# Kernel optimization log

Measured on AMD Instinct MI355X. Metric: run time of the kernel, lower is better.

Reference implementation:

```python
import jax, jax.numpy as jnp
import numpy as np

N_NODES = 4096
N_EDGES = 131072
C_IN = 256
C_OUT = 256
N_HEADS = 4
ALPHA = 0.2
NEG_FILL = -9e15


def setup_inputs() -> dict:
    key = jax.random.key(0)
    k_x, k_e, k_w, k_b, k_a = jax.random.split(key, 5)
    x = jax.random.normal(k_x, (N_NODES, C_IN), dtype=jnp.float32)
    edge_index = jax.random.randint(k_e, (2, N_EDGES), 0, N_NODES, dtype=jnp.int64)
    # nn.Linear(c_in, c_out): weight [c_out, c_in], bias [c_out]
    W = jax.random.normal(k_w, (C_OUT, C_IN), dtype=jnp.float32) * 0.05
    b = jax.random.normal(k_b, (C_OUT,), dtype=jnp.float32) * 0.05
    # attention vector a: [num_heads, 2 * c_out_per_head]
    a = jax.random.normal(k_a, (N_HEADS, 2 * (C_OUT // N_HEADS)), dtype=jnp.float32) * 0.05
    return {"x": x, "edge_index": edge_index, "W": W, "b": b, "a": a}


def reference(x, edge_index, W, b, a):
    N = x.shape[0]
    H = a.shape[0]
    C = W.shape[0] // H  # per-head feature dim

    # Linear projection then split heads: [N, H, C]
    feats = (x @ W.T + b).reshape(N, H, C)

    # Dense adjacency (faithful to the original index_select/scatter construction)
    adj = jnp.zeros((N, N), dtype=bool).at[edge_index[0], edge_index[1]].set(True)

    # attn_logits = leaky_relu(einsum('bhc,hc->bh', cat(f_i, f_j), a))
    # is separable: score(i,j,h) = leaky_relu(f_i . a[:, :C] + f_j . a[:, C:])
    s_src = jnp.einsum('nhc,hc->nh', feats, a[:, :C])  # [N, H]
    s_dst = jnp.einsum('nhc,hc->nh', feats, a[:, C:])  # [N, H]
    logits = jax.nn.leaky_relu(s_src[:, None, :] + s_dst[None, :, :], ALPHA)  # [N, N, H]

    masked = jnp.where(adj[..., None], logits, NEG_FILL)
    probs = jax.nn.softmax(masked, axis=1)  # softmax over source nodes j (dim=2 with batch)

    # Weighted aggregation: einsum('bijh,bjhc->bihc') then concat heads
    out = jnp.einsum('ijh,jhc->ihc', probs, feats).reshape(N, H * C)
    return out[None]  # [1, N, c_out] (batch_size = 1 in the original)
```

## Files before the change

kernel.cpp:

```cpp
#include <hip/hip_runtime.h>
#include <hip/hip_bf16.h>
#include <stdint.h>

#define N_NODES 4096
#define N_EDGES 131072
#define C_IN 256
#define C_OUT 256
#define N_HEADS 4
#define C_HEAD 64
#define MAX_DEG 128

typedef __attribute__((ext_vector_type(8))) short short8;
typedef __attribute__((ext_vector_type(4))) short short4v;
typedef __attribute__((ext_vector_type(4))) float floatx4;

union f32u { float f; uint32_t u; };
__device__ __forceinline__ float bf2f(short s) {
    f32u v; v.u = ((uint32_t)(uint16_t)s) << 16; return v.f;
}
__device__ __forceinline__ short f2bf(float f) {
    __hip_bfloat16 h = __float2bfloat16(f);
    return *reinterpret_cast<short*>(&h);
}

__global__ void scatter_edges(const int* __restrict__ ei,
                              unsigned short* __restrict__ nbr,
                              int* __restrict__ deg) {
    int e = blockIdx.x * blockDim.x + threadIdx.x;
    if (e >= N_EDGES) return;
    bool is64 = true;
    #pragma unroll
    for (int q = 1; q < 64; q += 2) is64 = is64 && (ei[q] == 0);
    int row, col;
    if (is64) {
        const long long* e64 = (const long long*)ei;
        row = (int)e64[e];
        col = (int)e64[N_EDGES + e];
    } else {
        row = ei[e];
        col = ei[N_EDGES + e];
    }
    int pos = atomicAdd(&deg[row], 1);
    if (pos < MAX_DEG) nbr[row * MAX_DEG + pos] = (unsigned short)col;
}

__global__ __launch_bounds__(256) void gemm_feats(
    const float* __restrict__ x, const float* __restrict__ W,
    const float* __restrict__ b, __hip_bfloat16* __restrict__ feats)
{
    int tid  = threadIdx.x;
    int lane = tid & 63;
    int wave = tid >> 6;
    int tile = blockIdx.x * 4 + wave;
    int row0 = (tile >> 4) * 16;
    int col0 = (tile & 15) * 16;
    int r    = lane & 15;
    int quad = lane >> 4;

    const floatx4* ax = (const floatx4*)(x + (size_t)(row0 + r) * C_IN);
    const floatx4* bw = (const floatx4*)(W + (size_t)(col0 + r) * C_IN);

    floatx4 acc = {0.f, 0.f, 0.f, 0.f};
    #pragma unroll
    for (int k8 = 0; k8 < 8; ++k8) {
        floatx4 a0 = ax[k8 * 8 + quad * 2], a1 = ax[k8 * 8 + quad * 2 + 1];
        floatx4 b0 = bw[k8 * 8 + quad * 2], b1 = bw[k8 * 8 + quad * 2 + 1];
        short8 av, bq;
        #pragma unroll
        for (int j = 0; j < 4; ++j) {
            av[j] = f2bf(a0[j]); av[4 + j] = f2bf(a1[j]);
            bq[j] = f2bf(b0[j]); bq[4 + j] = f2bf(b1[j]);
        }
        acc = __builtin_amdgcn_mfma_f32_16x16x32_bf16(av, bq, acc, 0, 0, 0);
    }

    int gn = col0 + r;
    float bias = b[gn];
    #pragma unroll
    for (int rr = 0; rr < 4; ++rr) {
        int gm = row0 + quad * 4 + rr;
        feats[(size_t)gm * C_OUT + gn] = __float2bfloat16(acc[rr] + bias);
    }
}

__global__ __launch_bounds__(64) void score_kernel(
    const __hip_bfloat16* __restrict__ feats, const float* __restrict__ a,
    float* __restrict__ s_src, float* __restrict__ s_dst)
{
    int gid = blockIdx.x * 64 + threadIdx.x;
    int n = gid >> 2, h = gid & 3;
    const short8*  f  = (const short8*)(feats + (size_t)n * C_OUT + h * C_HEAD);
    const floatx4* as = (const floatx4*)(a + h * 2 * C_HEAD);
    float ss = 0.f, sd = 0.f;
    #pragma unroll
    for (int v = 0; v < 8; ++v) {
        short8 fv = f[v];
        floatx4 s0 = as[v * 2],      s1 = as[v * 2 + 1];
        floatx4 d0 = as[16 + v * 2], d1 = as[16 + v * 2 + 1];
        #pragma unroll
        for (int j = 0; j < 4; ++j) {
            float x0 = bf2f(fv[j]);
            float x1 = bf2f(fv[4 + j]);
            ss += x0 * s0[j] + x1 * s1[j];
            sd += x0 * d0[j] + x1 * d1[j];
        }
    }
    s_src[gid] = ss;
    s_dst[gid] = sd;
}

__global__ __launch_bounds__(256) void aggregate(
    const unsigned short* __restrict__ nbr,
    const int* __restrict__ deg,
    const __hip_bfloat16* __restrict__ feats,
    const float* __restrict__ s_src,
    const float* __restrict__ s_dst,
    float* __restrict__ out)
{
    int i    = blockIdx.x;
    int t    = threadIdx.x;
    int wv   = t >> 6;
    int lane = t & 63;
    int h    = lane >> 4;

    __shared__ unsigned short lst[MAX_DEG];
    __shared__ unsigned char  ok[MAX_DEG];
    __shared__ float          wk[MAX_DEG][N_HEADS];
    __shared__ floatx4        red[4][64];

    int n = deg[i];
    n = (n < MAX_DEG) ? n : MAX_DEG;

    if (t < n) lst[t] = nbr[i * MAX_DEG + t];
    __syncthreads();
    if (t < n) {
        unsigned short v = lst[t];
        bool keep = true;
        for (int q = 0; q < t; ++q) keep = keep && (lst[q] != v);
        ok[t] = keep ? 1 : 0;
    }
    __syncthreads();
    for (int p = t; p < n * N_HEADS; p += 256) {
        int k = p >> 2, hh = p & 3;
        float l = s_src[i * N_HEADS + hh] + s_dst[(int)lst[k] * N_HEADS + hh];
        l = (l > 0.f) ? l : 0.2f * l;
        l = fminf(l, 60.f);
        wk[k][hh] = ok[k] ? __expf(l) : 0.f;
    }
    __syncthreads();

    floatx4 acc = {0.f, 0.f, 0.f, 0.f};
    if (n > 0) {
        for (int k = wv; k < n; k += 4) {
            float w = wk[k][h];
            short4v fv = *(const short4v*)(feats + (size_t)lst[k] * C_OUT + lane * 4);
            acc[0] += w * bf2f(fv[0]);
            acc[1] += w * bf2f(fv[1]);
            acc[2] += w * bf2f(fv[2]);
            acc[3] += w * bf2f(fv[3]);
        }
    } else {
        for (int j = wv; j < N_NODES; j += 4) {
            short4v fv = *(const short4v*)(feats + (size_t)j * C_OUT + lane * 4);
            acc[0] += bf2f(fv[0]);
            acc[1] += bf2f(fv[1]);
            acc[2] += bf2f(fv[2]);
            acc[3] += bf2f(fv[3]);
        }
    }
    red[wv][lane] = acc;
    __syncthreads();

    if (wv == 0) {
        floatx4 r0 = red[0][lane], r1 = red[1][lane], r2 = red[2][lane], r3 = red[3][lane];
        float denom;
        if (n > 0) {
            denom = 0.f;
            for (int k = 0; k < n; ++k) denom += wk[k][h];
            if (denom <= 0.f) denom = 1.f;
        } else {
            denom = (float)N_NODES;
        }
        float inv = 1.0f / denom;
        floatx4 o;
        o[0] = (r0[0] + r1[0] + r2[0] + r3[0]) * inv;
        o[1] = (r0[1] + r1[1] + r2[1] + r3[1]) * inv;
        o[2] = (r0[2] + r1[2] + r2[2] + r3[2]) * inv;
        o[3] = (r0[3] + r1[3] + r2[3] + r3[3]) * inv;
        *(floatx4*)(out + (size_t)i * C_OUT + lane * 4) = o;
    }
}

extern "C" void kernel_launch(void* const* d_in, const int* in_sizes, int n_in,
                              void* d_out, int out_size, void* d_ws, size_t ws_size,
                              hipStream_t stream) {
    const float* x  = (const float*)d_in[0];
    const int*   ei = (const int*)d_in[1];
    const float* W  = (const float*)d_in[2];
    const float* b  = (const float*)d_in[3];
    const float* a  = (const float*)d_in[4];
    float* out = (float*)d_out;

    uint8_t* ws = (uint8_t*)d_ws;
    __hip_bfloat16* feats = (__hip_bfloat16*)ws;
    unsigned short* nbr   = (unsigned short*)(ws + (2u << 20));
    int*            deg   = (int*)(ws + (3u << 20));
    float*          s_src = (float*)(ws + (3u << 20) + (16u << 10));
    float*          s_dst = (float*)(ws + (3u << 20) + (80u << 10));

    hipMemsetAsync(deg, 0, N_NODES * sizeof(int), stream);
    scatter_edges<<<N_EDGES / 256, 256, 0, stream>>>(ei, nbr, deg);
    gemm_feats<<<(N_NODES / 16) * (C_OUT / 16) / 4, 256, 0, stream>>>(x, W, b, feats);
    score_kernel<<<N_NODES * N_HEADS / 64, 64, 0, stream>>>(feats, a, s_src, s_dst);
    aggregate<<<N_NODES, 256, 0, stream>>>(nbr, deg, feats, s_src, s_dst, out);
}
```

Before: 111.2 us.

## Fuse GEMM with edge scatter and compute attention scores inside aggregation

Merges the edge-scatter and projection GEMM into one launch by splitting the block range between the two roles, with scatter blocks handling four edges per thread. The separate score kernel and its s_src/s_dst buffers are removed; the aggregate kernel now computes destination scores on the fly from the neighbour feature rows it already loads, using 16-lane shuffle reductions. The softmax denominator is accumulated per wave instead of in a serial loop over shared weights. This cuts two kernel launches and the shared-memory weight pass, at the cost of extra shuffles and dot products in the gather loop.

```diff
diff --git a/kernel.cpp b/kernel.cpp
--- a/kernel.cpp
+++ b/kernel.cpp
@@ -9,6 +9,8 @@
 #define N_HEADS 4
 #define C_HEAD 64
 #define MAX_DEG 128
+#define GEMM_BLOCKS 1024
+#define SCAT_BLOCKS 128
 
 typedef __attribute__((ext_vector_type(8))) short short8;
 typedef __attribute__((ext_vector_type(4))) short short4v;
@@ -23,98 +25,74 @@
     return *reinterpret_cast<short*>(&h);
 }
 
-__global__ void scatter_edges(const int* __restrict__ ei,
-                              unsigned short* __restrict__ nbr,
-                              int* __restrict__ deg) {
-    int e = blockIdx.x * blockDim.x + threadIdx.x;
-    if (e >= N_EDGES) return;
-    bool is64 = true;
-    #pragma unroll
-    for (int q = 1; q < 64; q += 2) is64 = is64 && (ei[q] == 0);
-    int row, col;
-    if (is64) {
-        const long long* e64 = (const long long*)ei;
-        row = (int)e64[e];
-        col = (int)e64[N_EDGES + e];
+__global__ __launch_bounds__(256) void k1_gemm_scatter(
+    const float* __restrict__ x, const float* __restrict__ W,
+    const float* __restrict__ b, const int* __restrict__ ei,
+    unsigned short* __restrict__ nbr, int* __restrict__ deg,
+    __hip_bfloat16* __restrict__ feats)
+{
+    int blk = blockIdx.x;
+    int tid = threadIdx.x;
+    if (blk < GEMM_BLOCKS) {
+        int lane = tid & 63;
+        int wave = tid >> 6;
+        int tile = blk * 4 + wave;
+        int row0 = (tile >> 4) * 16;
+        int col0 = (tile & 15) * 16;
+        int r    = lane & 15;
+        int quad = lane >> 4;
+
+        const floatx4* ax = (const floatx4*)(x + (size_t)(row0 + r) * C_IN);
+        const floatx4* bw = (const floatx4*)(W + (size_t)(col0 + r) * C_IN);
+
+        floatx4 acc = {0.f, 0.f, 0.f, 0.f};
+        #pragma unroll
+        for (int k8 = 0; k8 < 8; ++k8) {
+            floatx4 a0 = ax[k8 * 8 + quad * 2], a1 = ax[k8 * 8 + quad * 2 + 1];
+            floatx4 b0 = bw[k8 * 8 + quad * 2], b1 = bw[k8 * 8 + quad * 2 + 1];
+            short8 av, bq;
+            #pragma unroll
+            for (int j = 0; j < 4; ++j) {
+                av[j] = f2bf(a0[j]); av[4 + j] = f2bf(a1[j]);
+                bq[j] = f2bf(b0[j]); bq[4 + j] = f2bf(b1[j]);
+            }
+            acc = __builtin_amdgcn_mfma_f32_16x16x32_bf16(av, bq, acc, 0, 0, 0);
+        }
+        int gn = col0 + r;
+        float bias = b[gn];
+        #pragma unroll
+        for (int rr = 0; rr < 4; ++rr) {
+            int gm = row0 + quad * 4 + rr;
+            feats[(size_t)gm * C_OUT + gn] = __float2bfloat16(acc[rr] + bias);
+        }
     } else {
-        row = ei[e];
-        col = ei[N_EDGES + e];
-    }
-    int pos = atomicAdd(&deg[row], 1);
-    if (pos < MAX_DEG) nbr[row * MAX_DEG + pos] = (unsigned short)col;
-}
-
-__global__ __launch_bounds__(256) void gemm_feats(
-    const float* __restrict__ x, const float* __restrict__ W,
-    const float* __restrict__ b, __hip_bfloat16* __restrict__ feats)
-{
-    int tid  = threadIdx.x;
-    int lane = tid & 63;
-    int wave = tid >> 6;
-    int tile = blockIdx.x * 4 + wave;
-    int row0 = (tile >> 4) * 16;
-    int col0 = (tile & 15) * 16;
-    int r    = lane & 15;
-    int quad = lane >> 4;
-
-    const floatx4* ax = (const floatx4*)(x + (size_t)(row0 + r) * C_IN);
-    const floatx4* bw = (const floatx4*)(W + (size_t)(col0 + r) * C_IN);
-
-    floatx4 acc = {0.f, 0.f, 0.f, 0.f};
-    #pragma unroll
-    for (int k8 = 0; k8 < 8; ++k8) {
-        floatx4 a0 = ax[k8 * 8 + quad * 2], a1 = ax[k8 * 8 + quad * 2 + 1];
-        floatx4 b0 = bw[k8 * 8 + quad * 2], b1 = bw[k8 * 8 + quad * 2 + 1];
-        short8 av, bq;
-        #pragma unroll
-        for (int j = 0; j < 4; ++j) {
-            av[j] = f2bf(a0[j]); av[4 + j] = f2bf(a1[j]);
-            bq[j] = f2bf(b0[j]); bq[4 + j] = f2bf(b1[j]);
-        }
-        acc = __builtin_amdgcn_mfma_f32_16x16x32_bf16(av, bq, acc, 0, 0, 0);
-    }
-
-    int gn = col0 + r;
-    float bias = b[gn];
-    #pragma unroll
-    for (int rr = 0; rr < 4; ++rr) {
-        int gm = row0 + quad * 4 + rr;
-        feats[(size_t)gm * C_OUT + gn] = __float2bfloat16(acc[rr] + bias);
-    }
-}
-
-__global__ __launch_bounds__(64) void score_kernel(
-    const __hip_bfloat16* __restrict__ feats, const float* __restrict__ a,
-    float* __restrict__ s_src, float* __restrict__ s_dst)
-{
-    int gid = blockIdx.x * 64 + threadIdx.x;
-    int n = gid >> 2, h = gid & 3;
-    const short8*  f  = (const short8*)(feats + (size_t)n * C_OUT + h * C_HEAD);
-    const floatx4* as = (const floatx4*)(a + h * 2 * C_HEAD);
-    float ss = 0.f, sd = 0.f;
-    #pragma unroll
-    for (int v = 0; v < 8; ++v) {
-        short8 fv = f[v];
-        floatx4 s0 = as[v * 2],      s1 = as[v * 2 + 1];
-        floatx4 d0 = as[16 + v * 2], d1 = as[16 + v * 2 + 1];
-        #pragma unroll
-        for (int j = 0; j < 4; ++j) {
-            float x0 = bf2f(fv[j]);
-            float x1 = bf2f(fv[4 + j]);
-            ss += x0 * s0[j] + x1 * s1[j];
-            sd += x0 * d0[j] + x1 * d1[j];
-        }
-    }
-    s_src[gid] = ss;
-    s_dst[gid] = sd;
+        bool is64 = true;
+        #pragma unroll
+        for (int q = 1; q < 64; q += 2) is64 = is64 && (ei[q] == 0);
+        int base = (blk - GEMM_BLOCKS) * 256 + tid;
+        #pragma unroll
+        for (int qq = 0; qq < 4; ++qq) {
+            int e = base + qq * (SCAT_BLOCKS * 256);
+            int row, col;
+            if (is64) {
+                const long long* e64 = (const long long*)ei;
+                row = (int)e64[e];
+                col = (int)e64[N_EDGES + e];
+            } else {
+                row = ei[e];
+                col = ei[N_EDGES + e];
+            }
+            int pos = atomicAdd(&deg[row], 1);
+            if (pos < MAX_DEG) nbr[row * MAX_DEG + pos] = (unsigned short)col;
+        }
+    }
 }
 
 __global__ __launch_bounds__(256) void aggregate(
     const unsigned short* __restrict__ nbr,
     const int* __restrict__ deg,
     const __hip_bfloat16* __restrict__ feats,
-    const float* __restrict__ s_src,
-    const float* __restrict__ s_dst,
+    const float* __restrict__ a,
     float* __restrict__ out)
 {
     int i    = blockIdx.x;
@@ -122,11 +100,13 @@
     int wv   = t >> 6;
     int lane = t & 63;
     int h    = lane >> 4;
+    int li   = lane & 15;
 
     __shared__ unsigned short lst[MAX_DEG];
     __shared__ unsigned char  ok[MAX_DEG];
-    __shared__ float          wk[MAX_DEG][N_HEADS];
-    __shared__ floatx4        red[4][64];
+    __shared__ float          ssrc_sh[N_HEADS];
+    __shared__ floatx4        redv[4][64];
+    __shared__ float          redd[4][64];
 
     int n = deg[i];
     n = (n < MAX_DEG) ? n : MAX_DEG;
@@ -139,49 +119,59 @@
         for (int q = 0; q < t; ++q) keep = keep && (lst[q] != v);
         ok[t] = keep ? 1 : 0;
     }
+
+    floatx4 as4 = *(const floatx4*)(a + h * 2 * C_HEAD + 4 * li);
+    floatx4 ad4 = *(const floatx4*)(a + h * 2 * C_HEAD + C_HEAD + 4 * li);
+
+    if (wv == 0) {
+        short4v fi = *(const short4v*)(feats + (size_t)i * C_OUT + lane * 4);
+        float p = bf2f(fi[0]) * as4[0] + bf2f(fi[1]) * as4[1]
+                + bf2f(fi[2]) * as4[2] + bf2f(fi[3]) * as4[3];
+        p += __shfl_xor(p, 1, 16);
+        p += __shfl_xor(p, 2, 16);
+        p += __shfl_xor(p, 4, 16);
+        p += __shfl_xor(p, 8, 16);
+        if (li == 0) ssrc_sh[h] = p;
+    }
     __syncthreads();
-    for (int p = t; p < n * N_HEADS; p += 256) {
-        int k = p >> 2, hh = p & 3;
-        float l = s_src[i * N_HEADS + hh] + s_dst[(int)lst[k] * N_HEADS + hh];
-        l = (l > 0.f) ? l : 0.2f * l;
-        l = fminf(l, 60.f);
-        wk[k][hh] = ok[k] ? __expf(l) : 0.f;
-    }
-    __syncthreads();
-
+
+    float ssrc = ssrc_sh[h];
     floatx4 acc = {0.f, 0.f, 0.f, 0.f};
+    float   den = 0.f;
+
     if (n > 0) {
         for (int k = wv; k < n; k += 4) {
-            float w = wk[k][h];
-            short4v fv = *(const short4v*)(feats + (size_t)lst[k] * C_OUT + lane * 4);
-            acc[0] += w * bf2f(fv[0]);
-            acc[1] += w * bf2f(fv[1]);
-            acc[2] += w * bf2f(fv[2]);
-            acc[3] += w * bf2f(fv[3]);
+            int j = lst[k];
+            short4v fv = *(const short4v*)(feats + (size_t)j * C_OUT + lane * 4);
+            float f0 = bf2f(fv[0]), f1 = bf2f(fv[1]), f2 = bf2f(fv[2]), f3 = bf2f(fv[3]);
+            float p = f0 * ad4[0] + f1 * ad4[1] + f2 * ad4[2] + f3 * ad4[3];
+            p += __shfl_xor(p, 1, 16);
+            p += __shfl_xor(p, 2, 16);
+            p += __shfl_xor(p, 4, 16);
+            p += __shfl_xor(p, 8, 16);
+            float l = ssrc + p;
+            l = (l > 0.f) ? l : 0.2f * l;
+            float w = ok[k] ? __expf(fminf(l, 60.f)) : 0.f;
+            den += w;
+            acc[0] += w * f0; acc[1] += w * f1; acc[2] += w * f2; acc[3] += w * f3;
         }
     } else {
         for (int j = wv; j < N_NODES; j += 4) {
             short4v fv = *(const short4v*)(feats + (size_t)j * C_OUT + lane * 4);
-            acc[0] += bf2f(fv[0]);
-            acc[1] += bf2f(fv[1]);
-            acc[2] += bf2f(fv[2]);
-            acc[3] += bf2f(fv[3]);
-        }
-    }
-    red[wv][lane] = acc;
+            acc[0] += bf2f(fv[0]); acc[1] += bf2f(fv[1]);
+            acc[2] += bf2f(fv[2]); acc[3] += bf2f(fv[3]);
+            den += 1.0f;
+        }
+    }
+    redv[wv][lane] = acc;
+    redd[wv][lane] = den;
     __syncthreads();
 
     if (wv == 0) {
-        floatx4 r0 = red[0][lane], r1 = red[1][lane], r2 = red[2][lane], r3 = red[3][lane];
-        float denom;
-        if (n > 0) {
-            denom = 0.f;
-            for (int k = 0; k < n; ++k) denom += wk[k][h];
-            if (denom <= 0.f) denom = 1.f;
-        } else {
-            denom = (float)N_NODES;
-        }
-        float inv = 1.0f / denom;
+        floatx4 r0 = redv[0][lane], r1 = redv[1][lane], r2 = redv[2][lane], r3 = redv[3][lane];
+        float d = redd[0][lane] + redd[1][lane] + redd[2][lane] + redd[3][lane];
+        if (d <= 0.f) d = 1.f;
+        float inv = 1.0f / d;
         floatx4 o;
         o[0] = (r0[0] + r1[0] + r2[0] + r3[0]) * inv;
         o[1] = (r0[1] + r1[1] + r2[1] + r3[1]) * inv;
@@ -205,12 +195,8 @@
     __hip_bfloat16* feats = (__hip_bfloat16*)ws;
     unsigned short* nbr   = (unsigned short*)(ws + (2u << 20));
     int*            deg   = (int*)(ws + (3u << 20));
-    float*          s_src = (float*)(ws + (3u << 20) + (16u << 10));
-    float*          s_dst = (float*)(ws + (3u << 20) + (80u << 10));
 
     hipMemsetAsync(deg, 0, N_NODES * sizeof(int), stream);
-    scatter_edges<<<N_EDGES / 256, 256, 0, stream>>>(ei, nbr, deg);
-    gemm_feats<<<(N_NODES / 16) * (C_OUT / 16) / 4, 256, 0, stream>>>(x, W, b, feats);
-    score_kernel<<<N_NODES * N_HEADS / 64, 64, 0, stream>>>(feats, a, s_src, s_dst);
-    aggregate<<<N_NODES, 256, 0, stream>>>(nbr, deg, feats, s_src, s_dst, out);
-}
+    k1_gemm_scatter<<<GEMM_BLOCKS + SCAT_BLOCKS, 256, 0, stream>>>(x, W, b, ei, nbr, deg, feats);
+    aggregate<<<N_NODES, 256, 0, stream>>>(nbr, deg, feats, a, out);
+}
```

Result: faster. 108.6 us (-2.3%).
